# Optimization experiments

Hardware: AMD Instinct MI355X
Metric: run time of the kernel (lower is better)

Reference implementation:

```python
import jax, jax.numpy as jnp
import numpy as np

N_PATCH = 8      # patch_num = [8, 8]
N_BINS = 256     # histogram bins 0..255


def setup_inputs() -> dict:
    key = jax.random.key(0)
    k1, k2 = jax.random.split(key)
    sr = jax.random.uniform(k1, (16, 3, 1024, 1024), dtype=jnp.float32)
    hr = jax.random.uniform(k2, (16, 3, 1024, 1024), dtype=jnp.float32)
    return {"sr": sr, "hr": hr}


def _entropy_weight(hr):
    """Per-spatial-patch Shannon entropy of 8-bit histogram, broadcast to an
    [H, W] weight map, normalized as (w - w.min()) / w.max() (original w.max,
    matching torch evaluation order)."""
    B, C, H, W = hr.shape
    ph, pw = H // N_PATCH, W // N_PATCH
    # [64, B*C*ph*pw] — each patch covers the full batch+channel slice,
    # exactly as split_patch's img[..., i*ph:(i+1)*ph, j*pw:(j+1)*pw].
    patches = (hr.reshape(B, C, N_PATCH, ph, N_PATCH, pw)
                 .transpose(2, 4, 0, 1, 3, 5)
                 .reshape(N_PATCH * N_PATCH, -1))
    # (patch * 255).int() truncation; values in [0,1) -> bins 0..255
    vals = jnp.clip((patches * 255.0).astype(jnp.int32), 0, N_BINS - 1)
    counts = jax.vmap(lambda v: jnp.bincount(v, length=N_BINS))(vals)
    p = counts.astype(jnp.float32) / jnp.float32(vals.shape[1])  # density (unit bin width)
    safe_p = jnp.where(p > 0, p, 1.0)
    ent = -jnp.sum(jnp.where(p > 0, p * jnp.log2(safe_p), 0.0), axis=1)  # [64]
    # tile each patch's scalar entropy over its spatial block (row-major patch order)
    w = jnp.broadcast_to(ent.reshape(N_PATCH, 1, N_PATCH, 1),
                         (N_PATCH, ph, N_PATCH, pw)).reshape(H, W)
    w = (w - w.min()) / w.max()
    return w  # [H, W], broadcasts over B, C


def reference(sr, hr):
    w = _entropy_weight(hr)
    # L1 loss (mean reduction) on entropy-weighted images
    return jnp.mean(jnp.abs(w * sr - w * hr))
```

## Files before the change

### kernel.cpp

```cpp
#include <hip/hip_runtime.h>
#include <math.h>

#define NP      8
#define NBINS   256
#define BC      48
#define HH      1024
#define WW      1024
#define RPB     16
#define THREADS 256
#define NBLK1   3072
#define BLK_PER_I 384
#define PATCH_ELEMS (BC * 128 * 128)
#define N_TOTAL ((long long)BC * HH * WW)

#define GH_BYTES   ((size_t)NBLK1 * 2048 * 2)
#define GS_OFF     GH_BYTES
#define GS_BYTES   ((size_t)NBLK1 * NP * 4)
#define ENT_OFF    (GS_OFF + GS_BYTES)
#define ENT_BYTES  (64 * 8)
#define GT_OFF     (ENT_OFF + ENT_BYTES)
#define PATHA_BYTES (GT_OFF + 64 * 4)
#define B_GHIST_BYTES (64 * NBINS * 4)
#define B_GSUM_OFF    B_GHIST_BYTES
#define B_ENT_OFF     (B_GSUM_OFF + 256)

typedef float f4 __attribute__((ext_vector_type(4)));

__device__ __forceinline__ void load_g(const f4* __restrict__ s4,
                                       const f4* __restrict__ h4,
                                       int g, f4* sb, f4* hb)
{
#pragma unroll
    for (int k = 0; k < 2; ++k) {
        sb[k] = __builtin_nontemporal_load(&s4[(g * 2 + k) * (WW / 4)]);
        hb[k] = __builtin_nontemporal_load(&h4[(g * 2 + k) * (WW / 4)]);
    }
}

__device__ __forceinline__ void proc_g(const f4* sb, const f4* hb,
                                       float& acc, unsigned int* histj)
{
#pragma unroll
    for (int k = 0; k < 2; ++k) {
        f4 s = sb[k], h = hb[k];
#pragma unroll
        for (int e = 0; e < 4; ++e) {
            acc += fabsf(s[e] - h[e]);
            int b = min(max((int)(h[e] * 255.0f), 0), 255);
            atomicAdd(&histj[b], 1u);
        }
    }
}

template <bool ATOMIC>
__global__ __launch_bounds__(THREADS, 8)
void entrop_pass1(const float* __restrict__ sr, const float* __restrict__ hr,
                  unsigned int* __restrict__ gh32, float* __restrict__ gs)
{
    __shared__ unsigned int hist[NP * NBINS];
    const int t = threadIdx.x;
#pragma unroll
    for (int m = t; m < NP * NBINS; m += THREADS) hist[m] = 0;
    __syncthreads();

    const int r0 = blockIdx.x * RPB;
    const int i  = (r0 & (HH - 1)) >> 7;
    const int j  = t >> 5;
    unsigned int* histj = &hist[j << 8];

    const f4* s4 = (const f4*)sr + (size_t)r0 * (WW / 4) + t;
    const f4* h4 = (const f4*)hr + (size_t)r0 * (WW / 4) + t;

    float acc = 0.0f;
    f4 sA[2], hA[2], sB[2], hB[2];
    load_g(s4, h4, 0, sA, hA);
#pragma unroll
    for (int g = 0; g < 7; ++g) {
        if (g & 1) { load_g(s4, h4, g + 1, sA, hA); proc_g(sB, hB, acc, histj); }
        else       { load_g(s4, h4, g + 1, sB, hB); proc_g(sA, hA, acc, histj); }
    }
    proc_g(sB, hB, acc, histj);

    for (int off = 16; off; off >>= 1) acc += __shfl_down(acc, off, 32);
    if ((t & 31) == 0) {
        if (ATOMIC) atomicAdd(&gs[i * NP + j], acc);
        else        gs[blockIdx.x * NP + j] = acc;
    }

    __syncthreads();
    if (ATOMIC) {
        for (int m = t; m < NP * NBINS; m += THREADS) {
            unsigned int c = hist[m];
            if (c) atomicAdd(&gh32[i * NP * NBINS + m], c);
        }
    } else {
#pragma unroll
        for (int m = t; m < NP * NBINS / 2; m += THREADS)
            gh32[(size_t)blockIdx.x * (NP * NBINS / 2) + m] =
                hist[2 * m] | (hist[2 * m + 1] << 16);
    }
}

__global__ __launch_bounds__(THREADS)
void entrop_reduceA(const unsigned short* __restrict__ gh,
                    const float* __restrict__ gs,
                    double* __restrict__ ent, float* __restrict__ gsumT)
{
    const int p = blockIdx.x, i = p >> 3, jj = p & 7;
    const int t = threadIdx.x;

    unsigned int cnt = 0;
    const unsigned short* col = gh + jj * NBINS + t;
    for (int g = 0; g < BLK_PER_I / 8; ++g) {
#pragma unroll
        for (int d = 0; d < 8; ++d)
            cnt += col[(size_t)(64 * g + 8 * i + d) * 2048];
    }
    double term = 0.0;
    if (cnt) {
        double pd = (double)cnt * (1.0 / (double)PATCH_ELEMS);
        term = pd * log2(pd);
    }
    float sg = 0.0f;
    for (int idx = t; idx < BLK_PER_I; idx += THREADS) {
        int g = idx >> 3, d = idx & 7;
        sg += gs[(size_t)(64 * g + 8 * i + d) * NP + jj];
    }

    for (int off = 32; off; off >>= 1) {
        term += __shfl_down(term, off, 64);
        sg   += __shfl_down(sg, off, 64);
    }
    __shared__ double rd[4];
    __shared__ float  rf[4];
    if ((t & 63) == 0) { rd[t >> 6] = term; rf[t >> 6] = sg; }
    __syncthreads();
    if (t == 0) {
        ent[p]   = -(rd[0] + rd[1] + rd[2] + rd[3]);
        gsumT[p] = rf[0] + rf[1] + rf[2] + rf[3];
    }
}

__global__ __launch_bounds__(THREADS)
void entrop_reduceB(const unsigned int* __restrict__ ghist, double* __restrict__ ent)
{
    const int p = blockIdx.x, t = threadIdx.x;
    unsigned int c = ghist[p * NBINS + t];
    double term = 0.0;
    if (c) {
        double pd = (double)c * (1.0 / (double)PATCH_ELEMS);
        term = pd * log2(pd);
    }
    for (int off = 32; off; off >>= 1) term += __shfl_down(term, off, 64);
    __shared__ double rd[4];
    if ((t & 63) == 0) rd[t >> 6] = term;
    __syncthreads();
    if (t == 0) ent[p] = -(rd[0] + rd[1] + rd[2] + rd[3]);
}

__global__ void entrop_final(const double* __restrict__ ent,
                             const float* __restrict__ gsumT,
                             float* __restrict__ out)
{
    const int t = threadIdx.x;
    double e = ent[t];
    double mn = e, mx = e;
#pragma unroll
    for (int off = 32; off; off >>= 1) {
        mn = fmin(mn, __shfl_xor(mn, off, 64));
        mx = fmax(mx, __shfl_xor(mx, off, 64));
    }
    double contrib = (e - mn) / mx * (double)gsumT[t];
#pragma unroll
    for (int off = 32; off; off >>= 1) contrib += __shfl_xor(contrib, off, 64);
    if (t == 0) out[0] = (float)(contrib / (double)N_TOTAL);
}

extern "C" void kernel_launch(void* const* d_in, const int* in_sizes, int n_in,
                              void* d_out, int out_size, void* d_ws, size_t ws_size,
                              hipStream_t stream)
{
    const float* sr = (const float*)d_in[0];
    const float* hr = (const float*)d_in[1];
    float* out = (float*)d_out;
    char* ws = (char*)d_ws;

    if (ws_size >= PATHA_BYTES) {
        unsigned int*   gh32  = (unsigned int*)ws;
        float*          gs    = (float*)(ws + GS_OFF);
        double*         ent   = (double*)(ws + ENT_OFF);
        float*          gsumT = (float*)(ws + GT_OFF);
        entrop_pass1<false><<<NBLK1, THREADS, 0, stream>>>(sr, hr, gh32, gs);
        entrop_reduceA<<<64, THREADS, 0, stream>>>((const unsigned short*)gh32, gs, ent, gsumT);
        entrop_final<<<1, 64, 0, stream>>>(ent, gsumT, out);
    } else {
        unsigned int* ghist = (unsigned int*)ws;
        float*        gsum  = (float*)(ws + B_GSUM_OFF);
        double*       ent   = (double*)(ws + B_ENT_OFF);
        hipMemsetAsync(ws, 0, B_GSUM_OFF + 256, stream);
        entrop_pass1<true><<<NBLK1, THREADS, 0, stream>>>(sr, hr, ghist, gsum);
        entrop_reduceB<<<64, THREADS, 0, stream>>>(ghist, ent);
        entrop_final<<<1, 64, 0, stream>>>(ent, gsum, out);
    }
}
```

Before: 381.1 us.

## Stage input rows into LDS via async global_load_lds double buffering

The pass-1 kernel now copies groups of 4 rows of sr and hr straight into LDS using global_load_lds. It double-buffers these copies across groups so loads overlap the histogram and abs-diff work. Rows per block rise from 16 to 32, which halves the block count, and the reduce kernel's indexing is adjusted to match. This adds about 64KB of LDS per block and drops the occupancy hint, so fewer blocks can be resident on each CU. The histogram atomics stay the same, so they may still be the bottleneck.

New measurement: 401.2 us. 1.05x slower.

```diff
diff --git a/kernel.cpp b/kernel.cpp
--- a/kernel.cpp
+++ b/kernel.cpp
@@ -6,10 +6,13 @@
 #define BC      48
 #define HH      1024
 #define WW      1024
-#define RPB     16
+#define RPB     32
 #define THREADS 256
-#define NBLK1   3072
-#define BLK_PER_I 384
+#define NBLK1   1536
+#define BLK_PER_I 192
+#define U       4
+#define NG      (RPB / U)
+#define ROWB    4096
 #define PATCH_ELEMS (BC * 128 * 128)
 #define N_TOTAL ((long long)BC * HH * WW)
 
@@ -26,60 +29,77 @@
 
 typedef float f4 __attribute__((ext_vector_type(4)));
 
-__device__ __forceinline__ void load_g(const f4* __restrict__ s4,
-                                       const f4* __restrict__ h4,
-                                       int g, f4* sb, f4* hb)
-{
-#pragma unroll
-    for (int k = 0; k < 2; ++k) {
-        sb[k] = __builtin_nontemporal_load(&s4[(g * 2 + k) * (WW / 4)]);
-        hb[k] = __builtin_nontemporal_load(&h4[(g * 2 + k) * (WW / 4)]);
-    }
-}
-
-__device__ __forceinline__ void proc_g(const f4* sb, const f4* hb,
-                                       float& acc, unsigned int* histj)
-{
-#pragma unroll
-    for (int k = 0; k < 2; ++k) {
-        f4 s = sb[k], h = hb[k];
-#pragma unroll
-        for (int e = 0; e < 4; ++e) {
-            acc += fabsf(s[e] - h[e]);
-            int b = min(max((int)(h[e] * 255.0f), 0), 255);
-            atomicAdd(&histj[b], 1u);
+__device__ __forceinline__ void stage_group(const char* sr, const char* hr,
+                                            int grow, char* lds_buf,
+                                            int w, int lane)
+{
+    const char* gb = (w >> 1) ? hr : sr;
+    const int   ss = (w >> 1);
+    const int   u0 = (w & 1) * 2;
+#pragma unroll
+    for (int du = 0; du < 2; ++du) {
+        const int u = u0 + du;
+        const char* gp = gb + (size_t)(grow + u) * ROWB + (size_t)lane * 16;
+        char* lp = lds_buf + (ss * U + u) * ROWB;
+#pragma unroll
+        for (int c = 0; c < 4; ++c) {
+            __builtin_amdgcn_global_load_lds(
+                (const __attribute__((address_space(1))) void*)(gp + c * 1024),
+                (__attribute__((address_space(3))) void*)(lp + c * 1024),
+                16, 0, 0);
         }
     }
 }
 
 template <bool ATOMIC>
-__global__ __launch_bounds__(THREADS, 8)
+__global__ __launch_bounds__(THREADS)
 void entrop_pass1(const float* __restrict__ sr, const float* __restrict__ hr,
                   unsigned int* __restrict__ gh32, float* __restrict__ gs)
 {
+    __shared__ __align__(16) char ldsbuf[2][2 * U * ROWB];
     __shared__ unsigned int hist[NP * NBINS];
-    const int t = threadIdx.x;
+
+    const int t    = threadIdx.x;
+    const int w    = t >> 6;
+    const int lane = t & 63;
+    const int r0   = blockIdx.x * RPB;
+    const int i    = (r0 & (HH - 1)) >> 7;
+    const int j    = t >> 5;
+    unsigned int* histj = &hist[j << 8];
+
+    const char* sc = (const char*)sr;
+    const char* hc = (const char*)hr;
+
+    stage_group(sc, hc, r0, ldsbuf[0], w, lane);
 #pragma unroll
     for (int m = t; m < NP * NBINS; m += THREADS) hist[m] = 0;
     __syncthreads();
 
-    const int r0 = blockIdx.x * RPB;
-    const int i  = (r0 & (HH - 1)) >> 7;
-    const int j  = t >> 5;
-    unsigned int* histj = &hist[j << 8];
-
-    const f4* s4 = (const f4*)sr + (size_t)r0 * (WW / 4) + t;
-    const f4* h4 = (const f4*)hr + (size_t)r0 * (WW / 4) + t;
-
     float acc = 0.0f;
-    f4 sA[2], hA[2], sB[2], hB[2];
-    load_g(s4, h4, 0, sA, hA);
-#pragma unroll
-    for (int g = 0; g < 7; ++g) {
-        if (g & 1) { load_g(s4, h4, g + 1, sA, hA); proc_g(sB, hB, acc, histj); }
-        else       { load_g(s4, h4, g + 1, sB, hB); proc_g(sA, hA, acc, histj); }
-    }
-    proc_g(sB, hB, acc, histj);
+#pragma unroll 1
+    for (int g = 0; g < NG; ++g) {
+        if (g + 1 < NG) {
+            stage_group(sc, hc, r0 + (g + 1) * U, ldsbuf[(g + 1) & 1], w, lane);
+            asm volatile("s_waitcnt vmcnt(8)" ::: "memory");
+        } else {
+            asm volatile("s_waitcnt vmcnt(0)" ::: "memory");
+        }
+        __builtin_amdgcn_s_barrier();
+
+        const char* bs = ldsbuf[g & 1];
+#pragma unroll
+        for (int u = 0; u < U; ++u) {
+            f4 s = *(const f4*)(bs + u * ROWB + t * 16);
+            f4 h = *(const f4*)(bs + (U + u) * ROWB + t * 16);
+#pragma unroll
+            for (int e = 0; e < 4; ++e) {
+                acc += fabsf(s[e] - h[e]);
+                int b = min(max((int)(h[e] * 255.0f), 0), 255);
+                atomicAdd(&histj[b], 1u);
+            }
+        }
+        __builtin_amdgcn_s_barrier();
+    }
 
     for (int off = 16; off; off >>= 1) acc += __shfl_down(acc, off, 32);
     if ((t & 31) == 0) {
@@ -111,20 +131,24 @@
 
     unsigned int cnt = 0;
     const unsigned short* col = gh + jj * NBINS + t;
-    for (int g = 0; g < BLK_PER_I / 8; ++g) {
-#pragma unroll
-        for (int d = 0; d < 8; ++d)
-            cnt += col[(size_t)(64 * g + 8 * i + d) * 2048];
+#pragma unroll 1
+    for (int u = 0; u < 48; u += 4) {
+#pragma unroll
+        for (int v = 0; v < 4; ++v)
+#pragma unroll
+            for (int e = 0; e < 4; ++e)
+                cnt += col[(size_t)(32 * (u + v) + 4 * i + e) * 2048];
     }
     double term = 0.0;
     if (cnt) {
         double pd = (double)cnt * (1.0 / (double)PATCH_ELEMS);
         term = pd * log2(pd);
     }
+
     float sg = 0.0f;
-    for (int idx = t; idx < BLK_PER_I; idx += THREADS) {
-        int g = idx >> 3, d = idx & 7;
-        sg += gs[(size_t)(64 * g + 8 * i + d) * NP + jj];
+    if (t < BLK_PER_I) {
+        int u = t >> 2, e = t & 3;
+        sg = gs[(size_t)(32 * u + 4 * i + e) * NP + jj];
     }
 
     for (int off = 32; off; off >>= 1) {
```
